# Kernel tuning notes

Hardware: AMD Instinct MI355X
Metric: run time of the kernel (lower is better)

The kernel has to match this reference:

```python
import jax, jax.numpy as jnp
import numpy as np

S, B, T = 512, 256, 128


def setup_inputs() -> dict:
    key = jax.random.key(0)
    k_em, k_lab, k_s, k_t, k_e = jax.random.split(key, 5)
    emissions = jax.random.normal(k_em, (S, B, T), dtype=jnp.float32)
    labels = jax.random.randint(k_lab, (S, B), 0, T, dtype=jnp.int64)
    mask = jnp.ones((S, B), dtype=bool)
    starts = jax.random.uniform(k_s, (T,), minval=-0.1, maxval=0.1, dtype=jnp.float32)
    transitions = jax.random.uniform(k_t, (T, T), minval=-0.1, maxval=0.1, dtype=jnp.float32)
    ends = jax.random.uniform(k_e, (T,), minval=-0.1, maxval=0.1, dtype=jnp.float32)
    return {"emissions": emissions, "labels": labels, "mask": mask,
            "starts": starts, "transitions": transitions, "ends": ends}


def reference(emissions, labels, mask, starts, transitions, ends):
    # emissions: [S, B, T], labels/mask: [S, B]
    maskf = mask.astype(emissions.dtype)

    # ---- numerator: score of the gold path ----
    numerator = starts[labels[0]]  # [B]
    emit_scores = jnp.take_along_axis(emissions, labels[..., None], axis=2)[..., 0]  # [S, B]
    numerator += (emit_scores * maskf).sum(axis=0)
    trans_scores = transitions[labels[:-1], labels[1:]]  # [S-1, B]
    numerator += (trans_scores * maskf[1:]).sum(axis=0)
    seq_ends = mask.astype(jnp.int32).sum(axis=0) - 1  # [B]
    last_tags = jnp.take_along_axis(labels, seq_ends[None, :], axis=0)[0]  # [B]
    numerator += ends[last_tags]

    # ---- denominator: log partition via forward algorithm (scan) ----
    alpha0 = starts + emissions[0]  # [B, T]

    def step(alpha, inputs):
        em_i, mask_i = inputs  # em_i: [B, T], mask_i: [B]
        # alpha[b, i] + transitions[i, j] + em_i[b, j] -> logsumexp over i
        scores = alpha[:, :, None] + transitions[None, :, :] + em_i[:, None, :]
        nxt = jax.nn.logsumexp(scores, axis=1)  # [B, T]
        alpha = jnp.where(mask_i[:, None], nxt, alpha)
        return alpha, None

    alpha, _ = jax.lax.scan(step, alpha0, (emissions[1:], mask[1:]))
    denominator = jax.nn.logsumexp(alpha + ends, axis=1)  # [B]

    llh = numerator - denominator
    return -llh.sum() / maskf.sum()
```

## Files before the change

kernel.cpp:

```cpp
#include <hip/hip_runtime.h>

#define S_LEN 512
#define B_DIM 256
#define T_DIM 128
#define LOG2E 1.44269504088896340736f
#define LN2F  0.69314718055994530942f

typedef float v2f __attribute__((ext_vector_type(2)));
typedef float v4f __attribute__((ext_vector_type(4)));

#if __has_builtin(__builtin_elementwise_fma)
#define V2FMA(a, b, c) __builtin_elementwise_fma((a), (b), (c))
#else
static __device__ __forceinline__ v2f V2FMA(v2f a, v2f b, v2f c) {
  v2f r; r[0] = fmaf(a[0], b[0], c[0]); r[1] = fmaf(a[1], b[1], c[1]); return r;
}
#endif

__device__ __forceinline__ float dpp_xor1(float x) {
  int y = __builtin_amdgcn_update_dpp(0, __float_as_int(x), 0xB1, 0xF, 0xF, true);
  return __int_as_float(y);
}
__device__ __forceinline__ float dpp_xor2(float x) {
  int y = __builtin_amdgcn_update_dpp(0, __float_as_int(x), 0x4E, 0xF, 0xF, true);
  return __int_as_float(y);
}
__device__ __forceinline__ float dpp_add_ror8(float x) {
  int y = __builtin_amdgcn_update_dpp(0, __float_as_int(x), 0x128, 0xF, 0xF, true);
  return x + __int_as_float(y);
}

__global__ __launch_bounds__(256, 1) void crf_scan_kernel(
    const float* __restrict__ em,
    const float* __restrict__ starts,
    const float* __restrict__ trans,
    const float* __restrict__ ends,
    float* __restrict__ vec_out,
    int* __restrict__ e_out)
{
  __shared__ alignas(16) float w_lds[2][192];
  __shared__ float red_lds[4];

  const int bid = blockIdx.x;
  const int b   = bid >> 1;
  const bool fw = (bid & 1) == 0;
  const int t  = threadIdx.x;
  const int m  = (t & 3) | ((t >> 1) & 4);
  const int kg = ((t >> 2) & 1) | ((t >> 4) << 1);
  const int c  = 2 * (t & 1) + ((t >> 1) & 1);
  const int k_lane = 4 * kg + c;
  const int rbase  = 24 * m;
  const int wword  = k_lane + 4 * (k_lane >> 3);
  const bool writer = (t & 8) == 0;
  const size_t BT = (size_t)B_DIM * T_DIM;
  const float* em_sc = em + (size_t)b * T_DIM + k_lane;

  v2f E2[4][8];
  if (fw) {
#pragma unroll
    for (int q = 0; q < 8; ++q) {
      const float* r0 = &trans[(size_t)(16 * m + 2 * q) * T_DIM + 4 * kg];
      v4f ta = *reinterpret_cast<const v4f*>(r0);
      v4f tb = *reinterpret_cast<const v4f*>(r0 + T_DIM);
#pragma unroll
      for (int cc = 0; cc < 4; ++cc) {
        E2[cc][q][0] = __expf(ta[cc]);
        E2[cc][q][1] = __expf(tb[cc]);
      }
    }
  } else {
#pragma unroll
    for (int cc = 0; cc < 4; ++cc) {
      const float* r = &trans[(size_t)(4 * kg + cc) * T_DIM + 16 * m];
#pragma unroll
      for (int h = 0; h < 4; ++h) {
        v4f tv = *reinterpret_cast<const v4f*>(r + 4 * h);
        E2[cc][2 * h + 0][0] = __expf(tv[0]);
        E2[cc][2 * h + 0][1] = __expf(tv[1]);
        E2[cc][2 * h + 1][0] = __expf(tv[2]);
        E2[cc][2 * h + 1][1] = __expf(tv[3]);
      }
    }
  }

  {
    float wi = fw ? __expf(starts[k_lane] + em_sc[0])
                  : __expf(em_sc[(size_t)(S_LEN - 1) * BT] + ends[k_lane]);
    if (writer) w_lds[0][wword] = wi;
  }

  const int ds = fw ? 1 : -1;
  const int sA = fw ? 1 : (S_LEN - 2);
  float emr0 = em_sc[(size_t)(sA + 0 * ds) * BT];
  float emr1 = em_sc[(size_t)(sA + 1 * ds) * BT];
  float emr2 = em_sc[(size_t)(sA + 2 * ds) * BT];
  float emr3 = em_sc[(size_t)(sA + 3 * ds) * BT];

  int e_sum = 0, e_use = 0;
  int cur = 0;
  float wlast = 0.f;
  const bool b0 = (t & 1) != 0;
  const bool b1 = (t & 2) != 0;
  const int s_lo = fw ? 0 : 256;
  const int s_hi = fw ? 255 : S_LEN - 1;

  asm volatile("s_waitcnt lgkmcnt(0)" ::: "memory");
  __builtin_amdgcn_s_barrier();

  auto step = [&](float& emslot, int s_pref) {
    const v4f* wp = reinterpret_cast<const v4f*>(&w_lds[cur][rbase]);
    v4f wv0 = wp[0];
    v4f wv1 = wp[1];
    v4f wv2 = wp[3];
    v4f wv3 = wp[4];
    float w0 = w_lds[cur][0];

    e_sum += e_use;
    float f = __builtin_amdgcn_exp2f(fmaf(emslot, LOG2E, (float)(-e_use)));

    v2f p0 = __builtin_shufflevector(wv0, wv0, 0, 1);
    v2f p1 = __builtin_shufflevector(wv0, wv0, 2, 3);
    v2f p2 = __builtin_shufflevector(wv1, wv1, 0, 1);
    v2f p3 = __builtin_shufflevector(wv1, wv1, 2, 3);
    v2f p4 = __builtin_shufflevector(wv2, wv2, 0, 1);
    v2f p5 = __builtin_shufflevector(wv2, wv2, 2, 3);
    v2f p6 = __builtin_shufflevector(wv3, wv3, 0, 1);
    v2f p7 = __builtin_shufflevector(wv3, wv3, 2, 3);

    v2f A0 = (v2f){0.f, 0.f}, A1 = (v2f){0.f, 0.f};
    v2f A2 = (v2f){0.f, 0.f}, A3 = (v2f){0.f, 0.f};
#define PK(q)                                                                \
    A0 = V2FMA(p##q, E2[0][q], A0); A1 = V2FMA(p##q, E2[1][q], A1);          \
    A2 = V2FMA(p##q, E2[2][q], A2); A3 = V2FMA(p##q, E2[3][q], A3);
    PK(0) PK(1) PK(2) PK(3) PK(4) PK(5) PK(6) PK(7)
#undef PK
    float a0 = A0[0] + A0[1];
    float a1 = A1[0] + A1[1];
    float a2 = A2[0] + A2[1];
    float a3 = A3[0] + A3[1];

    float u = b0 ? a0 : a2;
    float v = b0 ? a1 : a3;
    u = dpp_xor1(u);
    v = dpp_xor1(v);
    float x = (b0 ? a2 : a0) + u;
    float y = (b0 ? a3 : a1) + v;
    float s2 = b1 ? x : y;
    s2 = dpp_xor2(s2);
    float z = (b1 ? y : x) + s2;
    z = dpp_add_ror8(z);

    z *= f;
    if (writer) w_lds[cur ^ 1][wword] = z;
    wlast = z;

    e_use = (int)((__float_as_uint(w0) >> 23) & 0xFF) - 127;

    int sf = s_pref < s_lo ? s_lo : (s_pref > s_hi ? s_hi : s_pref);
    emslot = em_sc[(size_t)sf * BT];

    asm volatile("s_waitcnt lgkmcnt(0)" ::: "memory");
    __builtin_amdgcn_s_barrier();
    cur ^= 1;
  };

  int s0 = sA;
  for (int it = 0; it < 63; ++it) {
    step(emr0, s0 + 4 * ds);
    step(emr1, s0 + 5 * ds);
    step(emr2, s0 + 6 * ds);
    step(emr3, s0 + 7 * ds);
    s0 += 4 * ds;
  }
  step(emr0, s_hi);
  step(emr1, s_hi);
  step(emr2, s_hi);

  if (fw) {
    const v4f* wp = reinterpret_cast<const v4f*>(&w_lds[cur][rbase]);
    v4f wv0 = wp[0];
    v4f wv1 = wp[1];
    v4f wv2 = wp[3];
    v4f wv3 = wp[4];
    e_sum += e_use;
    float f = __builtin_amdgcn_exp2f((float)(-e_use));
    v2f p0 = __builtin_shufflevector(wv0, wv0, 0, 1);
    v2f p1 = __builtin_shufflevector(wv0, wv0, 2, 3);
    v2f p2 = __builtin_shufflevector(wv1, wv1, 0, 1);
    v2f p3 = __builtin_shufflevector(wv1, wv1, 2, 3);
    v2f p4 = __builtin_shufflevector(wv2, wv2, 0, 1);
    v2f p5 = __builtin_shufflevector(wv2, wv2, 2, 3);
    v2f p6 = __builtin_shufflevector(wv3, wv3, 0, 1);
    v2f p7 = __builtin_shufflevector(wv3, wv3, 2, 3);
    v2f A0 = (v2f){0.f, 0.f}, A1 = (v2f){0.f, 0.f};
    v2f A2 = (v2f){0.f, 0.f}, A3 = (v2f){0.f, 0.f};
#define PK(q)                                                                \
    A0 = V2FMA(p##q, E2[0][q], A0); A1 = V2FMA(p##q, E2[1][q], A1);          \
    A2 = V2FMA(p##q, E2[2][q], A2); A3 = V2FMA(p##q, E2[3][q], A3);
    PK(0) PK(1) PK(2) PK(3) PK(4) PK(5) PK(6) PK(7)
#undef PK
    float a0 = A0[0] + A0[1];
    float a1 = A1[0] + A1[1];
    float a2 = A2[0] + A2[1];
    float a3 = A3[0] + A3[1];
    float u = b0 ? a0 : a2;
    float v = b0 ? a1 : a3;
    u = dpp_xor1(u);
    v = dpp_xor1(v);
    float x = (b0 ? a2 : a0) + u;
    float y = (b0 ? a3 : a1) + v;
    float s2 = b1 ? x : y;
    s2 = dpp_xor2(s2);
    float z = (b1 ? y : x) + s2;
    z = dpp_add_ror8(z);
    wlast = z * f;
  }

  if (writer)
    vec_out[((size_t)(fw ? 0 : 1) * B_DIM + b) * T_DIM + k_lane] = wlast;
  if (t == 0)
    e_out[(fw ? 0 : 1) * B_DIM + b] = e_sum;
}

__global__ __launch_bounds__(128, 1) void crf_combine_kernel(
    const float* __restrict__ vec,
    const int* __restrict__ es,
    float* __restrict__ den_out)
{
  const int b = blockIdx.x;
  const int t = threadIdx.x;
  float p = vec[(size_t)b * T_DIM + t] *
            vec[((size_t)B_DIM + b) * T_DIM + t];
#pragma unroll
  for (int off = 32; off > 0; off >>= 1) p += __shfl_down(p, off, 64);
  __shared__ float rs[2];
  if ((t & 63) == 0) rs[t >> 6] = p;
  __syncthreads();
  if (t == 0)
    den_out[b] = (float)(es[b] + es[B_DIM + b]) * LN2F + __logf(rs[0] + rs[1]);
}

__global__ __launch_bounds__(256, 1) void crf_num_kernel(
    const float* __restrict__ em,
    const int* __restrict__ labels32,
    const float* __restrict__ starts,
    const float* __restrict__ trans,
    const float* __restrict__ ends,
    float* __restrict__ num_out)
{
  const int b = blockIdx.x;
  const int t = threadIdx.x;

  __shared__ int scale_sh;
  if (t < 64) {
    int v = labels32[2 * t + 1];
    unsigned long long any = __ballot(v != 0);
    if (t == 0) scale_sh = (any == 0ULL) ? 2 : 1;
  }
  __syncthreads();
  const int scale = scale_sh;

  float partial = 0.f;
  for (int s = t; s < S_LEN; s += 256) {
    int lab = labels32[(size_t)(s * B_DIM + b) * scale];
    partial += em[(size_t)s * B_DIM * T_DIM + (size_t)b * T_DIM + lab];
    if (s > 0) {
      int labp = labels32[(size_t)((s - 1) * B_DIM + b) * scale];
      partial += trans[labp * T_DIM + lab];
    }
  }
#pragma unroll
  for (int off = 32; off > 0; off >>= 1) partial += __shfl_down(partial, off, 64);
  __shared__ float fred[4];
  if ((t & 63) == 0) fred[t >> 6] = partial;
  __syncthreads();
  if (t == 0) {
    float sum = fred[0] + fred[1] + fred[2] + fred[3];
    sum += starts[labels32[(size_t)b * scale]];
    sum += ends[labels32[(size_t)((S_LEN - 1) * B_DIM + b) * scale]];
    num_out[b] = sum;
  }
}

__global__ void crf_final_kernel(const float* __restrict__ den,
                                 const float* __restrict__ num,
                                 float* __restrict__ out)
{
  int t = threadIdx.x;
  float d = den[t] - num[t];
#pragma unroll
  for (int off = 32; off > 0; off >>= 1) d += __shfl_down(d, off, 64);
  __shared__ float rd[4];
  if ((t & 63) == 0) rd[t >> 6] = d;
  __syncthreads();
  if (t == 0) out[0] = (rd[0] + rd[1] + rd[2] + rd[3]) / (float)(S_LEN * B_DIM);
}

extern "C" void kernel_launch(void* const* d_in, const int* in_sizes, int n_in,
                              void* d_out, int out_size, void* d_ws, size_t ws_size,
                              hipStream_t stream) {
  const float* em      = (const float*)d_in[0];
  const int*   labels  = (const int*)d_in[1];
  const float* starts  = (const float*)d_in[3];
  const float* trans   = (const float*)d_in[4];
  const float* ends    = (const float*)d_in[5];
  float* out = (float*)d_out;

  float* den = (float*)d_ws;
  float* num = den + B_DIM;
  float* vec = num + B_DIM;
  int*   es  = (int*)(vec + 2 * B_DIM * T_DIM);

  crf_scan_kernel<<<2 * B_DIM, 256, 0, stream>>>(em, starts, trans, ends, vec, es);
  crf_num_kernel<<<B_DIM, 256, 0, stream>>>(em, labels, starts, trans, ends, num);
  crf_combine_kernel<<<B_DIM, 128, 0, stream>>>(vec, es, den);
  crf_final_kernel<<<1, 256, 0, stream>>>(den, num, out);
}
```

Measured before the change: 94.65 us.

## Halve scan block to 128 threads with 8 outputs per lane

The forward/backward CRF scan block shrinks from 256 to 128 threads (two wavefronts). Each lane now covers a 16x8 tile of the transition matrix instead of 16x4, so it holds 64 packed exp-transition registers and eight accumulators. The cross-lane reduction is reorganised so that every lane writes its own output, which removes the duplicated writer lanes. The aim is to reduce per-step barrier and LDS-traffic overhead in the latency-bound sequential scan, at the cost of more FMAs and higher register pressure per lane.

```diff
diff --git a/kernel.cpp b/kernel.cpp
--- a/kernel.cpp
+++ b/kernel.cpp
@@ -25,12 +25,12 @@
   int y = __builtin_amdgcn_update_dpp(0, __float_as_int(x), 0x4E, 0xF, 0xF, true);
   return __int_as_float(y);
 }
-__device__ __forceinline__ float dpp_add_ror8(float x) {
+__device__ __forceinline__ float dpp_ror8(float x) {
   int y = __builtin_amdgcn_update_dpp(0, __float_as_int(x), 0x128, 0xF, 0xF, true);
-  return x + __int_as_float(y);
-}
-
-__global__ __launch_bounds__(256, 1) void crf_scan_kernel(
+  return __int_as_float(y);
+}
+
+__global__ __launch_bounds__(128, 1) void crf_scan_kernel(
     const float* __restrict__ em,
     const float* __restrict__ starts,
     const float* __restrict__ trans,
@@ -38,47 +38,45 @@
     float* __restrict__ vec_out,
     int* __restrict__ e_out)
 {
-  __shared__ alignas(16) float w_lds[2][192];
-  __shared__ float red_lds[4];
+  __shared__ alignas(16) float w_lds[2][160];
 
   const int bid = blockIdx.x;
   const int b   = bid >> 1;
   const bool fw = (bid & 1) == 0;
   const int t  = threadIdx.x;
-  const int m  = (t & 3) | ((t >> 1) & 4);
+  const int gl = (t & 3) | ((t >> 1) & 4);
   const int kg = ((t >> 2) & 1) | ((t >> 4) << 1);
-  const int c  = 2 * (t & 1) + ((t >> 1) & 1);
-  const int k_lane = 4 * kg + c;
-  const int rbase  = 24 * m;
-  const int wword  = k_lane + 4 * (k_lane >> 3);
-  const bool writer = (t & 8) == 0;
+  const int c  = 4 * (t & 1) + 2 * ((t >> 1) & 1) + ((t >> 3) & 1);
+  const int k_lane = 8 * kg + c;
+  const int rbase  = 20 * gl;
+  const int wword  = k_lane + 4 * (k_lane >> 4);
   const size_t BT = (size_t)B_DIM * T_DIM;
   const float* em_sc = em + (size_t)b * T_DIM + k_lane;
 
-  v2f E2[4][8];
+  v2f E2[8][8];
   if (fw) {
 #pragma unroll
-    for (int q = 0; q < 8; ++q) {
-      const float* r0 = &trans[(size_t)(16 * m + 2 * q) * T_DIM + 4 * kg];
-      v4f ta = *reinterpret_cast<const v4f*>(r0);
-      v4f tb = *reinterpret_cast<const v4f*>(r0 + T_DIM);
-#pragma unroll
-      for (int cc = 0; cc < 4; ++cc) {
-        E2[cc][q][0] = __expf(ta[cc]);
-        E2[cc][q][1] = __expf(tb[cc]);
+    for (int jj = 0; jj < 16; ++jj) {
+      const float* r = &trans[(size_t)(16 * gl + jj) * T_DIM + 8 * kg];
+      v4f ta = *reinterpret_cast<const v4f*>(r);
+      v4f tb = *reinterpret_cast<const v4f*>(r + 4);
+#pragma unroll
+      for (int a = 0; a < 4; ++a) {
+        E2[a][jj >> 1][jj & 1]     = __expf(ta[a]);
+        E2[a + 4][jj >> 1][jj & 1] = __expf(tb[a]);
       }
     }
   } else {
 #pragma unroll
-    for (int cc = 0; cc < 4; ++cc) {
-      const float* r = &trans[(size_t)(4 * kg + cc) * T_DIM + 16 * m];
+    for (int a = 0; a < 8; ++a) {
+      const float* r = &trans[(size_t)(8 * kg + a) * T_DIM + 16 * gl];
 #pragma unroll
       for (int h = 0; h < 4; ++h) {
         v4f tv = *reinterpret_cast<const v4f*>(r + 4 * h);
-        E2[cc][2 * h + 0][0] = __expf(tv[0]);
-        E2[cc][2 * h + 0][1] = __expf(tv[1]);
-        E2[cc][2 * h + 1][0] = __expf(tv[2]);
-        E2[cc][2 * h + 1][1] = __expf(tv[3]);
+        E2[a][2 * h + 0][0] = __expf(tv[0]);
+        E2[a][2 * h + 0][1] = __expf(tv[1]);
+        E2[a][2 * h + 1][0] = __expf(tv[2]);
+        E2[a][2 * h + 1][1] = __expf(tv[3]);
       }
     }
   }
@@ -86,7 +84,7 @@
   {
     float wi = fw ? __expf(starts[k_lane] + em_sc[0])
                   : __expf(em_sc[(size_t)(S_LEN - 1) * BT] + ends[k_lane]);
-    if (writer) w_lds[0][wword] = wi;
+    w_lds[0][wword] = wi;
   }
 
   const int ds = fw ? 1 : -1;
@@ -101,6 +99,7 @@
   float wlast = 0.f;
   const bool b0 = (t & 1) != 0;
   const bool b1 = (t & 2) != 0;
+  const bool b3 = (t & 8) != 0;
   const int s_lo = fw ? 0 : 256;
   const int s_hi = fw ? 255 : S_LEN - 1;
 
@@ -111,8 +110,8 @@
     const v4f* wp = reinterpret_cast<const v4f*>(&w_lds[cur][rbase]);
     v4f wv0 = wp[0];
     v4f wv1 = wp[1];
-    v4f wv2 = wp[3];
-    v4f wv3 = wp[4];
+    v4f wv2 = wp[2];
+    v4f wv3 = wp[3];
     float w0 = w_lds[cur][0];
 
     e_sum += e_use;
@@ -129,29 +128,48 @@
 
     v2f A0 = (v2f){0.f, 0.f}, A1 = (v2f){0.f, 0.f};
     v2f A2 = (v2f){0.f, 0.f}, A3 = (v2f){0.f, 0.f};
+    v2f A4 = (v2f){0.f, 0.f}, A5 = (v2f){0.f, 0.f};
+    v2f A6 = (v2f){0.f, 0.f}, A7 = (v2f){0.f, 0.f};
 #define PK(q)                                                                \
     A0 = V2FMA(p##q, E2[0][q], A0); A1 = V2FMA(p##q, E2[1][q], A1);          \
-    A2 = V2FMA(p##q, E2[2][q], A2); A3 = V2FMA(p##q, E2[3][q], A3);
+    A2 = V2FMA(p##q, E2[2][q], A2); A3 = V2FMA(p##q, E2[3][q], A3);          \
+    A4 = V2FMA(p##q, E2[4][q], A4); A5 = V2FMA(p##q, E2[5][q], A5);          \
+    A6 = V2FMA(p##q, E2[6][q], A6); A7 = V2FMA(p##q, E2[7][q], A7);
     PK(0) PK(1) PK(2) PK(3) PK(4) PK(5) PK(6) PK(7)
 #undef PK
-    float a0 = A0[0] + A0[1];
-    float a1 = A1[0] + A1[1];
-    float a2 = A2[0] + A2[1];
-    float a3 = A3[0] + A3[1];
-
-    float u = b0 ? a0 : a2;
-    float v = b0 ? a1 : a3;
-    u = dpp_xor1(u);
-    v = dpp_xor1(v);
-    float x = (b0 ? a2 : a0) + u;
-    float y = (b0 ? a3 : a1) + v;
-    float s2 = b1 ? x : y;
-    s2 = dpp_xor2(s2);
-    float z = (b1 ? y : x) + s2;
-    z = dpp_add_ror8(z);
+    float h0 = A0[0] + A0[1];
+    float h1 = A1[0] + A1[1];
+    float h2 = A2[0] + A2[1];
+    float h3 = A3[0] + A3[1];
+    float h4 = A4[0] + A4[1];
+    float h5 = A5[0] + A5[1];
+    float h6 = A6[0] + A6[1];
+    float h7 = A7[0] + A7[1];
+
+    float u0 = b0 ? h0 : h4;
+    float u1 = b0 ? h1 : h5;
+    float u2 = b0 ? h2 : h6;
+    float u3 = b0 ? h3 : h7;
+    u0 = dpp_xor1(u0);
+    u1 = dpp_xor1(u1);
+    u2 = dpp_xor1(u2);
+    u3 = dpp_xor1(u3);
+    float x0 = (b0 ? h4 : h0) + u0;
+    float x1 = (b0 ? h5 : h1) + u1;
+    float x2 = (b0 ? h6 : h2) + u2;
+    float x3 = (b0 ? h7 : h3) + u3;
+    float s0 = b1 ? x0 : x2;
+    float s1 = b1 ? x1 : x3;
+    s0 = dpp_xor2(s0);
+    s1 = dpp_xor2(s1);
+    float y0 = (b1 ? x2 : x0) + s0;
+    float y1 = (b1 ? x3 : x1) + s1;
+    float rr = b3 ? y0 : y1;
+    rr = dpp_ror8(rr);
+    float z = (b3 ? y1 : y0) + rr;
 
     z *= f;
-    if (writer) w_lds[cur ^ 1][wword] = z;
+    w_lds[cur ^ 1][wword] = z;
     wlast = z;
 
     e_use = (int)((__float_as_uint(w0) >> 23) & 0xFF) - 127;
@@ -164,13 +182,13 @@
     cur ^= 1;
   };
 
-  int s0 = sA;
+  int s0i = sA;
   for (int it = 0; it < 63; ++it) {
-    step(emr0, s0 + 4 * ds);
-    step(emr1, s0 + 5 * ds);
-    step(emr2, s0 + 6 * ds);
-    step(emr3, s0 + 7 * ds);
-    s0 += 4 * ds;
+    step(emr0, s0i + 4 * ds);
+    step(emr1, s0i + 5 * ds);
+    step(emr2, s0i + 6 * ds);
+    step(emr3, s0i + 7 * ds);
+    s0i += 4 * ds;
   }
   step(emr0, s_hi);
   step(emr1, s_hi);
@@ -180,8 +198,8 @@
     const v4f* wp = reinterpret_cast<const v4f*>(&w_lds[cur][rbase]);
     v4f wv0 = wp[0];
     v4f wv1 = wp[1];
-    v4f wv2 = wp[3];
-    v4f wv3 = wp[4];
+    v4f wv2 = wp[2];
+    v4f wv3 = wp[3];
     e_sum += e_use;
     float f = __builtin_amdgcn_exp2f((float)(-e_use));
     v2f p0 = __builtin_shufflevector(wv0, wv0, 0, 1);
@@ -194,30 +212,48 @@
     v2f p7 = __builtin_shufflevector(wv3, wv3, 2, 3);
     v2f A0 = (v2f){0.f, 0.f}, A1 = (v2f){0.f, 0.f};
     v2f A2 = (v2f){0.f, 0.f}, A3 = (v2f){0.f, 0.f};
+    v2f A4 = (v2f){0.f, 0.f}, A5 = (v2f){0.f, 0.f};
+    v2f A6 = (v2f){0.f, 0.f}, A7 = (v2f){0.f, 0.f};
 #define PK(q)                                                                \
     A0 = V2FMA(p##q, E2[0][q], A0); A1 = V2FMA(p##q, E2[1][q], A1);          \
-    A2 = V2FMA(p##q, E2[2][q], A2); A3 = V2FMA(p##q, E2[3][q], A3);
+    A2 = V2FMA(p##q, E2[2][q], A2); A3 = V2FMA(p##q, E2[3][q], A3);          \
+    A4 = V2FMA(p##q, E2[4][q], A4); A5 = V2FMA(p##q, E2[5][q], A5);          \
+    A6 = V2FMA(p##q, E2[6][q], A6); A7 = V2FMA(p##q, E2[7][q], A7);
     PK(0) PK(1) PK(2) PK(3) PK(4) PK(5) PK(6) PK(7)
 #undef PK
-    float a0 = A0[0] + A0[1];
-    float a1 = A1[0] + A1[1];
-    float a2 = A2[0] + A2[1];
-    float a3 = A3[0] + A3[1];
-    float u = b0 ? a0 : a2;
-    float v = b0 ? a1 : a3;
-    u = dpp_xor1(u);
-    v = dpp_xor1(v);
-    float x = (b0 ? a2 : a0) + u;
-    float y = (b0 ? a3 : a1) + v;
-    float s2 = b1 ? x : y;
-    s2 = dpp_xor2(s2);
-    float z = (b1 ? y : x) + s2;
-    z = dpp_add_ror8(z);
+    float h0 = A0[0] + A0[1];
+    float h1 = A1[0] + A1[1];
+    float h2 = A2[0] + A2[1];
+    float h3 = A3[0] + A3[1];
+    float h4 = A4[0] + A4[1];
+    float h5 = A5[0] + A5[1];
+    float h6 = A6[0] + A6[1];
+    float h7 = A7[0] + A7[1];
+    float u0 = b0 ? h0 : h4;
+    float u1 = b0 ? h1 : h5;
+    float u2 = b0 ? h2 : h6;
+    float u3 = b0 ? h3 : h7;
+    u0 = dpp_xor1(u0);
+    u1 = dpp_xor1(u1);
+    u2 = dpp_xor1(u2);
+    u3 = dpp_xor1(u3);
+    float x0 = (b0 ? h4 : h0) + u0;
+    float x1 = (b0 ? h5 : h1) + u1;
+    float x2 = (b0 ? h6 : h2) + u2;
+    float x3 = (b0 ? h7 : h3) + u3;
+    float s0 = b1 ? x0 : x2;
+    float s1 = b1 ? x1 : x3;
+    s0 = dpp_xor2(s0);
+    s1 = dpp_xor2(s1);
+    float y0 = (b1 ? x2 : x0) + s0;
+    float y1 = (b1 ? x3 : x1) + s1;
+    float rr = b3 ? y0 : y1;
+    rr = dpp_ror8(rr);
+    float z = (b3 ? y1 : y0) + rr;
     wlast = z * f;
   }
 
-  if (writer)
-    vec_out[((size_t)(fw ? 0 : 1) * B_DIM + b) * T_DIM + k_lane] = wlast;
+  vec_out[((size_t)(fw ? 0 : 1) * B_DIM + b) * T_DIM + k_lane] = wlast;
   if (t == 0)
     e_out[(fw ? 0 : 1) * B_DIM + b] = e_sum;
 }
@@ -311,7 +347,7 @@
   float* vec = num + B_DIM;
   int*   es  = (int*)(vec + 2 * B_DIM * T_DIM);
 
-  crf_scan_kernel<<<2 * B_DIM, 256, 0, stream>>>(em, starts, trans, ends, vec, es);
+  crf_scan_kernel<<<2 * B_DIM, 128, 0, stream>>>(em, starts, trans, ends, vec, es);
   crf_num_kernel<<<B_DIM, 256, 0, stream>>>(em, labels, starts, trans, ends, num);
   crf_combine_kernel<<<B_DIM, 128, 0, stream>>>(vec, es, den);
   crf_final_kernel<<<1, 256, 0, stream>>>(den, num, out);
```

Result: slower. 139.9 us (+47.8%).
